# Kernel tuning notes

Measured on AMD Instinct MI355X. Metric: run time of the kernel, lower is better.

The kernel has to match this reference:

```python
import jax, jax.numpy as jnp
import numpy as np

B, S, D, H = 2, 2048, 1024, 16
HD = D // H          # 64
NREF = HD // 2       # 32 Householder reflections
BLOCK = 128          # flex_attention block granularity
ROPE_BASE = 10000.0


def setup_inputs() -> dict:
    key = jax.random.key(0)
    ks = jax.random.split(key, 12)
    x = jax.random.normal(ks[0], (B, S, D), jnp.float32)
    # block-causal block mask (flex_attention block_mask analogue)
    nb = S // BLOCK
    bm = jnp.tril(jnp.ones((nb, nb), bool))
    mask = jnp.repeat(jnp.repeat(bm, BLOCK, axis=0), BLOCK, axis=1)  # [S,S]
    s = lambda fan: fan ** -0.5
    vs = jax.random.normal(ks[1], (NREF, HD), jnp.float32) * 0.02
    w_qkv = jax.random.normal(ks[2], (D, 3 * D), jnp.float32) * s(D)
    w_out = jax.random.normal(ks[3], (D, D), jnp.float32) * s(D)
    w_gate = jax.random.normal(ks[4], (D, D), jnp.float32) * s(D)
    b_gate = jnp.zeros((D,), jnp.float32)
    w_mlp_gate = jax.random.normal(ks[5], (D, 8 * D), jnp.float32) * s(D)
    b_mlp_gate = jnp.zeros((8 * D,), jnp.float32)
    w_mlp_out = jax.random.normal(ks[6], (4 * D, D), jnp.float32) * s(4 * D)
    b_mlp_out = jnp.zeros((D,), jnp.float32)
    return dict(x=x, mask=mask, grid_size=S, vs=vs, w_qkv=w_qkv, w_out=w_out,
                w_gate=w_gate, b_gate=b_gate, w_mlp_gate=w_mlp_gate,
                b_mlp_gate=b_mlp_gate, w_mlp_out=w_mlp_out, b_mlp_out=b_mlp_out)


def rmsnorm(x):
    return x * jax.lax.rsqrt(jnp.mean(x * x, axis=-1, keepdims=True) + 1e-6)


def householder_matrix(vs):
    # Q = prod_i (I - 2 v_i v_i^T / |v_i|^2), applied sequentially as in torch loop
    def body(Q, v):
        vn = jnp.sum(v * v) + 1e-8
        return Q - (2.0 / vn) * jnp.outer(v, v @ Q), None
    Q0 = jnp.eye(HD, dtype=vs.dtype)
    Q, _ = jax.lax.scan(body, Q0, vs)
    return Q


def rope_tables(seq_len, dtype):
    inv_freq = 1.0 / (ROPE_BASE ** (jnp.arange(0, HD, 2, dtype=jnp.float32) / HD))
    ang = jnp.arange(seq_len, dtype=jnp.float32)[:, None] * inv_freq  # [S, HD/2]
    ang = jnp.concatenate([ang, ang], axis=-1)                        # [S, HD]
    return jnp.cos(ang).astype(dtype), jnp.sin(ang).astype(dtype)


def rotate_half(x):
    x1, x2 = jnp.split(x, 2, axis=-1)
    return jnp.concatenate([-x2, x1], axis=-1)


def reference(x, mask, grid_size, vs, w_qkv, w_out, w_gate, b_gate,
              w_mlp_gate, b_mlp_gate, w_mlp_out, b_mlp_out):
    del grid_size  # positions derived from sequence length
    resid = x
    h = rmsnorm(x)
    qkv = h @ w_qkv                                # [B,S,3D]
    q, k, v = jnp.split(qkv, 3, axis=-1)
    to_heads = lambda t: t.reshape(B, S, H, HD).transpose(0, 2, 1, 3)  # [B,H,S,hd]
    q, k, v = to_heads(q), to_heads(k), to_heads(v)

    # RnRoPE: inverse Householder rotation, rope, forward Householder rotation
    Q = householder_matrix(vs)                     # [hd,hd]
    q = q @ Q.T
    k = k @ Q.T
    cos, sin = rope_tables(S, x.dtype)             # [S,hd]
    cos = cos[None, None]; sin = sin[None, None]
    q = q * cos + rotate_half(q) * sin
    k = k * cos + rotate_half(k) * sin
    q = q @ Q
    k = k @ Q

    # block-sparse attention (mask realized as boolean [S,S])
    scores = jnp.einsum('bhqd,bhkd->bhqk', q, k) / jnp.sqrt(jnp.asarray(HD, x.dtype))
    scores = jnp.where(mask[None, None], scores, jnp.asarray(-1e30, x.dtype))
    attn = jnp.einsum('bhqk,bhkd->bhqd', jax.nn.softmax(scores, axis=-1), v)
    attn = attn.transpose(0, 2, 1, 3).reshape(B, S, D)
    attn = attn @ w_out

    gate = jax.nn.sigmoid(attn @ w_gate + b_gate)
    x = resid + attn * gate

    resid = x
    gv = rmsnorm(x) @ w_mlp_gate + b_mlp_gate      # [B,S,8D]
    g, val = jnp.split(gv, 2, axis=-1)
    x = resid + (val * jax.nn.gelu(g, approximate=False)) @ w_mlp_out + b_mlp_out
    return x
```

## Files before the change

### kernel.cpp

```cpp
#include <hip/hip_runtime.h>
#include <hip/hip_bf16.h>
#include <math.h>

#define BT 2
#define SEQ 2048
#define DIM 1024
#define NH 16
#define HD 64
#define NTOK (BT*SEQ)

typedef __attribute__((ext_vector_type(4))) float floatx4;
typedef __attribute__((ext_vector_type(8))) short shortx8;
typedef __attribute__((ext_vector_type(4))) short shortx4;

#define GLL16(gp, lp) __builtin_amdgcn_global_load_lds( \
    (const __attribute__((address_space(1))) unsigned int*)(const void*)(gp), \
    (__attribute__((address_space(3))) unsigned int*)(void*)(lp), 16, 0, 0)

__device__ __forceinline__ float bf2f(unsigned short u) {
    unsigned int x = ((unsigned int)u) << 16;
    return __builtin_bit_cast(float, x);
}
__device__ __forceinline__ unsigned short f2bf(float f) {
    unsigned int x = __builtin_bit_cast(unsigned int, f);
    unsigned int lsb = (x >> 16) & 1u;
    x += 0x7fffu + lsb;
    return (unsigned short)(x >> 16);
}
__device__ __forceinline__ float ldin_f(const void* p, size_t i, int isbf) {
    return isbf ? bf2f(((const unsigned short*)p)[i]) : ((const float*)p)[i];
}

__global__ void detect_kernel(const unsigned short* __restrict__ x, int* __restrict__ flag) {
    __shared__ int cnt;
    if (threadIdx.x == 0) cnt = 0;
    __syncthreads();
    unsigned short u = x[(size_t)threadIdx.x * 2];
    int e = (u >> 7) & 0xFF;
    if (e >= 100 && e <= 140) atomicAdd(&cnt, 1);
    __syncthreads();
    if (threadIdx.x == 0) *flag = (cnt >= 192) ? 1 : 0;
}

__global__ void transpose_any(const void* __restrict__ in,
                              unsigned short* __restrict__ out, int R, int C,
                              const int* __restrict__ flagp) {
    int isbf = *flagp;
    __shared__ unsigned short tile[32][33];
    int c0 = blockIdx.x * 32, r0 = blockIdx.y * 32;
    int tx = threadIdx.x, ty = threadIdx.y;
#pragma unroll
    for (int i = 0; i < 4; i++) {
        size_t idx = (size_t)(r0 + ty + i * 8) * C + c0 + tx;
        tile[ty + i * 8][tx] = isbf ? ((const unsigned short*)in)[idx]
                                    : f2bf(((const float*)in)[idx]);
    }
    __syncthreads();
#pragma unroll
    for (int i = 0; i < 4; i++)
        out[(size_t)(c0 + ty + i * 8) * R + r0 + tx] = tile[tx][ty + i * 8];
}

__global__ __launch_bounds__(64) void householder_kernel(const void* __restrict__ vs,
                                                         float* __restrict__ Qg,
                                                         const int* __restrict__ flagp) {
    int isbf = *flagp;
    __shared__ float vsh[64];
    int j = threadIdx.x;
    float Qc[64];
#pragma unroll
    for (int i = 0; i < 64; i++) Qc[i] = (i == j) ? 1.f : 0.f;
    for (int r = 0; r < 32; r++) {
        vsh[j] = ldin_f(vs, r * 64 + j, isbf);
        __syncthreads();
        float va[64];
#pragma unroll
        for (int i = 0; i < 64; i++) va[i] = vsh[i];
        float vn0 = 0.f, vn1 = 0.f, vn2 = 0.f, vn3 = 0.f;
        float t0 = 0.f, t1 = 0.f, t2 = 0.f, t3 = 0.f;
#pragma unroll
        for (int i = 0; i < 16; i++) {
            vn0 += va[4 * i + 0] * va[4 * i + 0];
            vn1 += va[4 * i + 1] * va[4 * i + 1];
            vn2 += va[4 * i + 2] * va[4 * i + 2];
            vn3 += va[4 * i + 3] * va[4 * i + 3];
            t0 += va[4 * i + 0] * Qc[4 * i + 0];
            t1 += va[4 * i + 1] * Qc[4 * i + 1];
            t2 += va[4 * i + 2] * Qc[4 * i + 2];
            t3 += va[4 * i + 3] * Qc[4 * i + 3];
        }
        float vn = (vn0 + vn1) + (vn2 + vn3) + 1e-8f;
        float t = (t0 + t1) + (t2 + t3);
        float c = (2.f / vn) * t;
#pragma unroll
        for (int i = 0; i < 64; i++) Qc[i] -= c * va[i];
        __syncthreads();
    }
#pragma unroll
    for (int i = 0; i < 64; i++) Qg[i * 64 + j] = Qc[i];
}

__global__ __launch_bounds__(256) void rotate_wqkv(unsigned short* __restrict__ wT,
                                                   const float* __restrict__ Qg) {
    __shared__ float Qs[64][64];
    __shared__ unsigned short tile[64][128];
    int bid = blockIdx.x;
    int row0 = (bid >> 3) * 64;
    int col0 = (bid & 7) * 128;
    int t = threadIdx.x;
#pragma unroll
    for (int i = 0; i < 16; i++) {
        int idx = i * 256 + t;
        Qs[idx >> 6][idx & 63] = Qg[idx];
    }
#pragma unroll
    for (int i = 0; i < 8; i++) {
        int e = i * 256 + t;
        int r = e >> 5, cg = (e & 31) * 4;
        *(shortx4*)&tile[r][cg] = *(const shortx4*)&wT[(size_t)(row0 + r) * 1024 + col0 + cg];
    }
    __syncthreads();
    int ib = t >> 5;
    int c = (t & 31) * 4;
    float acc[8][4];
#pragma unroll
    for (int rr = 0; rr < 8; rr++)
#pragma unroll
        for (int cx = 0; cx < 4; cx++) acc[rr][cx] = 0.f;
    for (int j = 0; j < 64; j++) {
        float t0 = bf2f(tile[j][c]);
        float t1 = bf2f(tile[j][c + 1]);
        float t2 = bf2f(tile[j][c + 2]);
        float t3 = bf2f(tile[j][c + 3]);
#pragma unroll
        for (int rr = 0; rr < 8; rr++) {
            float qv = Qs[rr * 8 + ib][j];
            acc[rr][0] += qv * t0;
            acc[rr][1] += qv * t1;
            acc[rr][2] += qv * t2;
            acc[rr][3] += qv * t3;
        }
    }
#pragma unroll
    for (int rr = 0; rr < 8; rr++) {
        int i = rr * 8 + ib;
        shortx4 o4;
#pragma unroll
        for (int cx = 0; cx < 4; cx++) o4[cx] = (short)f2bf(acc[rr][cx]);
        *(shortx4*)&wT[(size_t)(row0 + i) * 1024 + col0 + c] = o4;
    }
}

__global__ void rope_table(float* __restrict__ tab) {
    int idx = blockIdx.x * 256 + threadIdx.x;
    int s = idx >> 5, fi = idx & 31;
    float invf = __expf(-(float)fi * (9.210340371976184f / 32.f));
    float ang = (float)s * invf;
    tab[2 * idx]     = cosf(ang);
    tab[2 * idx + 1] = sinf(ang);
}

__global__ __launch_bounds__(256) void rmsnorm2(const void* __restrict__ x,
                                                unsigned short* __restrict__ h,
                                                const int* __restrict__ flagp) {
    int isbf = flagp ? *flagp : 1;
    __shared__ float red[256];
    int row = blockIdx.x, t = threadIdx.x;
    size_t base = (size_t)row * DIM;
    float v[4];
    float ss = 0.f;
#pragma unroll
    for (int i = 0; i < 4; i++) {
        v[i] = ldin_f(x, base + t + 256 * i, isbf);
        ss += v[i] * v[i];
    }
    red[t] = ss;
    __syncthreads();
    for (int s = 128; s > 0; s >>= 1) {
        if (t < s) red[t] += red[t + s];
        __syncthreads();
    }
    float rs = rsqrtf(red[0] * (1.f / 1024.f) + 1e-6f);
#pragma unroll
    for (int i = 0; i < 4; i++) h[base + t + 256 * i] = f2bf(v[i] * rs);
}

template<int BN>
__global__ __launch_bounds__(256) void gemm_bt(const unsigned short* __restrict__ A,
                                               const unsigned short* __restrict__ Bt,
                                               void* __restrict__ C,
                                               const void* __restrict__ bias,
                                               const unsigned short* __restrict__ resid,
                                               const int* __restrict__ flagp,
                                               int M, int N, int K, int c_f32) {
    constexpr int NJ = BN / 32;
    __shared__ __align__(16) unsigned short As[2][128][32];
    __shared__ __align__(16) unsigned short Bs[2][BN][32];
    int bisbf = (bias && flagp) ? *flagp : 1;
    int tile = (blockIdx.x & 7) * (gridDim.x >> 3) + (blockIdx.x >> 3);
    int nbn = N / BN;
    int m0 = (tile / nbn) * 128;
    int n0 = (tile % nbn) * BN;
    int t = threadIdx.x;
    int lane = t & 63;
    int w = t >> 6;
    int wr = (w >> 1) * 64;
    int wc = (w & 1) * (16 * NJ);
    int lr = lane & 15;
    int kg = lane >> 4;

    floatx4 acc[4][NJ];
#pragma unroll
    for (int i = 0; i < 4; i++)
#pragma unroll
        for (int j = 0; j < NJ; j++) acc[i][j] = (floatx4){0.f, 0.f, 0.f, 0.f};

    int srow = w * 16 + (lane >> 2);
    int skseg = (lane & 3) * 8;
    const unsigned short* aP = A + (size_t)(m0 + srow) * K + skseg;
    const unsigned short* bP = Bt + (size_t)(n0 + srow) * K + skseg;
    size_t r64 = (size_t)64 * K;

    GLL16(aP,       &As[0][w * 16][0]);
    GLL16(aP + r64, &As[0][64 + w * 16][0]);
    GLL16(bP,       &Bs[0][w * 16][0]);
    if constexpr (BN == 128) GLL16(bP + r64, &Bs[0][64 + w * 16][0]);
    __syncthreads();

    int cur = 0;
    for (int k0 = 0; k0 < K; k0 += 32) {
        if (k0 + 32 < K) {
            int nb = cur ^ 1;
            GLL16(aP + k0 + 32,       &As[nb][w * 16][0]);
            GLL16(aP + r64 + k0 + 32, &As[nb][64 + w * 16][0]);
            GLL16(bP + k0 + 32,       &Bs[nb][w * 16][0]);
            if constexpr (BN == 128) GLL16(bP + r64 + k0 + 32, &Bs[nb][64 + w * 16][0]);
        }
        shortx8 af[4], bfv[NJ];
#pragma unroll
        for (int i = 0; i < 4; i++) af[i] = *(const shortx8*)&As[cur][wr + i * 16 + lr][kg * 8];
#pragma unroll
        for (int j = 0; j < NJ; j++) bfv[j] = *(const shortx8*)&Bs[cur][wc + j * 16 + lr][kg * 8];
#pragma unroll
        for (int i = 0; i < 4; i++)
#pragma unroll
            for (int j = 0; j < NJ; j++)
                acc[i][j] = __builtin_amdgcn_mfma_f32_16x16x32_bf16(af[i], bfv[j], acc[i][j], 0, 0, 0);
        __syncthreads();
        cur ^= 1;
    }
#pragma unroll
    for (int i = 0; i < 4; i++) {
#pragma unroll
        for (int j = 0; j < NJ; j++) {
            int col = n0 + wc + j * 16 + lr;
            int rbase = m0 + wr + i * 16 + kg * 4;
            float bv = bias ? ldin_f(bias, col, bisbf) : 0.f;
#pragma unroll
            for (int r = 0; r < 4; r++) {
                float val = acc[i][j][r] + bv;
                size_t oidx = (size_t)(rbase + r) * N + col;
                if (resid) val += bf2f(resid[oidx]);
                if (c_f32) ((float*)C)[oidx] = val;
                else       ((unsigned short*)C)[oidx] = f2bf(val);
            }
        }
    }
}

__global__ __launch_bounds__(256) void gemm_glu(const unsigned short* __restrict__ A,
                                                const unsigned short* __restrict__ Bt,
                                                unsigned short* __restrict__ act,
                                                const void* __restrict__ bias,
                                                const int* __restrict__ flagp) {
    __shared__ __align__(16) unsigned short As[2][128][32];
    __shared__ __align__(16) unsigned short Bg[2][64][32];
    __shared__ __align__(16) unsigned short Bv[2][64][32];
    const int K = 1024;
    int isbf = *flagp;
    int tile = (blockIdx.x & 7) * (gridDim.x >> 3) + (blockIdx.x >> 3);
    int m0 = (tile & 31) * 128;
    int n0 = (tile >> 5) * 64;
    int t = threadIdx.x;
    int lane = t & 63;
    int w = t >> 6;
    int wr = (w >> 1) * 64;
    int wc = (w & 1) * 32;
    int lr = lane & 15;
    int kg = lane >> 4;

    floatx4 ag[4][2], av[4][2];
#pragma unroll
    for (int i = 0; i < 4; i++)
#pragma unroll
        for (int j = 0; j < 2; j++) {
            ag[i][j] = (floatx4){0.f, 0.f, 0.f, 0.f};
            av[i][j] = (floatx4){0.f, 0.f, 0.f, 0.f};
        }

    int srow = w * 16 + (lane >> 2);
    int skseg = (lane & 3) * 8;
    const unsigned short* aP  = A + (size_t)(m0 + srow) * K + skseg;
    const unsigned short* bgP = Bt + (size_t)(n0 + srow) * K + skseg;
    const unsigned short* bvP = Bt + (size_t)(4096 + n0 + srow) * K + skseg;
    size_t r64 = (size_t)64 * K;

    GLL16(aP,       &As[0][w * 16][0]);
    GLL16(aP + r64, &As[0][64 + w * 16][0]);
    GLL16(bgP,      &Bg[0][w * 16][0]);
    GLL16(bvP,      &Bv[0][w * 16][0]);
    __syncthreads();

    int cur = 0;
    for (int k0 = 0; k0 < K; k0 += 32) {
        if (k0 + 32 < K) {
            int nb = cur ^ 1;
            GLL16(aP + k0 + 32,       &As[nb][w * 16][0]);
            GLL16(aP + r64 + k0 + 32, &As[nb][64 + w * 16][0]);
            GLL16(bgP + k0 + 32,      &Bg[nb][w * 16][0]);
            GLL16(bvP + k0 + 32,      &Bv[nb][w * 16][0]);
        }
        shortx8 af[4], gf[2], vf[2];
#pragma unroll
        for (int i = 0; i < 4; i++) af[i] = *(const shortx8*)&As[cur][wr + i * 16 + lr][kg * 8];
#pragma unroll
        for (int j = 0; j < 2; j++) {
            gf[j] = *(const shortx8*)&Bg[cur][wc + j * 16 + lr][kg * 8];
            vf[j] = *(const shortx8*)&Bv[cur][wc + j * 16 + lr][kg * 8];
        }
#pragma unroll
        for (int i = 0; i < 4; i++)
#pragma unroll
            for (int j = 0; j < 2; j++) {
                ag[i][j] = __builtin_amdgcn_mfma_f32_16x16x32_bf16(af[i], gf[j], ag[i][j], 0, 0, 0);
                av[i][j] = __builtin_amdgcn_mfma_f32_16x16x32_bf16(af[i], vf[j], av[i][j], 0, 0, 0);
            }
        __syncthreads();
        cur ^= 1;
    }
#pragma unroll
    for (int i = 0; i < 4; i++) {
#pragma unroll
        for (int j = 0; j < 2; j++) {
            int col = n0 + wc + j * 16 + lr;
            int rbase = m0 + wr + i * 16 + kg * 4;
            float bgv = ldin_f(bias, col, isbf);
            float bvv = ldin_f(bias, 4096 + col, isbf);
#pragma unroll
            for (int r = 0; r < 4; r++) {
                float g = ag[i][j][r] + bgv;
                float v = av[i][j][r] + bvv;
                float ge = 0.5f * g * (1.f + erff(g * 0.70710678118f));
                act[(size_t)(rbase + r) * 4096 + col] = f2bf(v * ge);
            }
        }
    }
}

__global__ __launch_bounds__(256) void qk_rope3(const unsigned short* __restrict__ qkv,
                                                const float* __restrict__ tab,
                                                unsigned short* __restrict__ q_r,
                                                unsigned short* __restrict__ k_r) {
    int tid = blockIdx.x * 256 + threadIdx.x;
    int c = tid & 3;
    int h = (tid >> 2) & 15;
    int ts = tid >> 6;
    int s = ts & 2047, b = ts >> 11;
    int d0 = c * 8;
    const unsigned short* base = qkv + (size_t)ts * 3072 + h * 64;
    shortx8 qlo = *(const shortx8*)(base + d0);
    shortx8 qhi = *(const shortx8*)(base + d0 + 32);
    shortx8 klo = *(const shortx8*)(base + 1024 + d0);
    shortx8 khi = *(const shortx8*)(base + 1024 + d0 + 32);
    const float* tp = tab + (size_t)s * 64 + d0 * 2;
    shortx8 oql, oqh, okl, okh;
#pragma unroll
    for (int i = 0; i < 8; i++) {
        float cv = tp[2 * i], sv = tp[2 * i + 1];
        float ql = bf2f((unsigned short)qlo[i]), qh = bf2f((unsigned short)qhi[i]);
        float kl = bf2f((unsigned short)klo[i]), kh = bf2f((unsigned short)khi[i]);
        oql[i] = (short)f2bf(ql * cv - qh * sv);
        oqh[i] = (short)f2bf(qh * cv + ql * sv);
        okl[i] = (short)f2bf(kl * cv - kh * sv);
        okh[i] = (short)f2bf(kh * cv + kl * sv);
    }
    size_t o = ((size_t)(b * NH + h) * SEQ + s) * HD + d0;
    *(shortx8*)(q_r + o)      = oql;
    *(shortx8*)(q_r + o + 32) = oqh;
    *(shortx8*)(k_r + o)      = okl;
    *(shortx8*)(k_r + o + 32) = okh;
}

__global__ __launch_bounds__(512) void attn_mfma(const unsigned short* __restrict__ q_r,
                                                 const unsigned short* __restrict__ k_r,
                                                 const unsigned short* __restrict__ qkv,
                                                 unsigned short* __restrict__ attn) {
    __shared__ __align__(16) unsigned short Ks[64][72];
    __shared__ __align__(16) unsigned short Vt[64 * 72];
    __shared__ __align__(16) unsigned short Ps[8][16][72];
    int bid = blockIdx.x;
    int qblk = 15 - (bid & 15);
    int bh = bid >> 4;
    int b = bh >> 4, h = bh & 15;
    size_t bh_off = (size_t)bh * SEQ * HD;
    int tid = threadIdx.x;
    int wv = tid >> 6, lane = tid & 63;
    int l16 = lane & 15, quad = lane >> 4;
    int q0 = qblk * 128 + wv * 16;

    const unsigned short* qrow = q_r + bh_off + (size_t)(q0 + l16) * HD + quad * 8;
    shortx8 aq0 = *(const shortx8*)(qrow);
    shortx8 aq1 = *(const shortx8*)(qrow + 32);

    floatx4 o[4];
#pragma unroll
    for (int nt = 0; nt < 4; nt++) o[nt] = (floatx4){0.f, 0.f, 0.f, 0.f};
    float m_run = -1e30f, l_run = 0.f;

    int nk = (qblk + 1) * 128;
    int skey = tid >> 3;
    int sd0 = (tid & 7) * 8;
    const unsigned short* kbase = k_r + bh_off + (size_t)skey * HD + sd0;
    const unsigned short* vbase = qkv + ((size_t)(b * SEQ + skey)) * 3072 + 2048 + h * 64 + sd0;
    int vco = (((skey >> 3) ^ (tid & 7)) * 8) + (skey & 7);

    shortx8 kv = *(const shortx8*)kbase;
    shortx8 vvv = *(const shortx8*)vbase;

    for (int k0 = 0; k0 < nk; k0 += 64) {
        __syncthreads();
        *(shortx8*)&Ks[skey][sd0] = kv;
#pragma unroll
        for (int i = 0; i < 8; i++) Vt[(size_t)(sd0 + i) * 72 + vco] = (unsigned short)vvv[i];
        __syncthreads();
        if (k0 + 64 < nk) {
            kv  = *(const shortx8*)(kbase + (size_t)(k0 + 64) * HD);
            vvv = *(const shortx8*)(vbase + (size_t)(k0 + 64) * 3072);
        }

        floatx4 sc[4];
#pragma unroll
        for (int kt = 0; kt < 4; kt++) {
            shortx8 bk0 = *(const shortx8*)&Ks[kt * 16 + l16][quad * 8];
            shortx8 bk1 = *(const shortx8*)&Ks[kt * 16 + l16][32 + quad * 8];
            floatx4 z = (floatx4){0.f, 0.f, 0.f, 0.f};
            z = __builtin_amdgcn_mfma_f32_16x16x32_bf16(bk0, aq0, z, 0, 0, 0);
            z = __builtin_amdgcn_mfma_f32_16x16x32_bf16(bk1, aq1, z, 0, 0, 0);
            sc[kt] = z;
        }
        float sv[16], mx[16];
#pragma unroll
        for (int kt = 0; kt < 4; kt++)
#pragma unroll
            for (int r = 0; r < 4; r++) sv[kt * 4 + r] = sc[kt][r] * 0.125f;
#pragma unroll
        for (int i = 0; i < 16; i++) mx[i] = sv[i];
#pragma unroll
        for (int st = 8; st > 0; st >>= 1)
#pragma unroll
            for (int i = 0; i < 8; i++)
                if (i < st) mx[i] = fmaxf(mx[i], mx[i + st]);
        float mt = mx[0];
        mt = fmaxf(mt, __shfl_xor(mt, 16, 64));
        mt = fmaxf(mt, __shfl_xor(mt, 32, 64));
        float nm = fmaxf(m_run, mt);
        float al = __expf(m_run - nm);
        m_run = nm;
        float p[16];
#pragma unroll
        for (int i = 0; i < 16; i++) p[i] = __expf(sv[i] - nm);
        float sm[8];
#pragma unroll
        for (int i = 0; i < 8; i++) sm[i] = p[i] + p[i + 8];
        float ps = ((sm[0] + sm[1]) + (sm[2] + sm[3])) + ((sm[4] + sm[5]) + (sm[6] + sm[7]));
        ps += __shfl_xor(ps, 16, 64);
        ps += __shfl_xor(ps, 32, 64);
        l_run = l_run * al + ps;
#pragma unroll
        for (int kt = 0; kt < 4; kt++) {
            shortx4 pk;
#pragma unroll
            for (int r = 0; r < 4; r++) pk[r] = (short)f2bf(p[kt * 4 + r]);
            *(shortx4*)&Ps[wv][l16][kt * 16 + quad * 4] = pk;
        }
#pragma unroll
        for (int r = 0; r < 4; r++) {
            float alr = __shfl(al, quad * 4 + r, 64);
            o[0][r] *= alr; o[1][r] *= alr; o[2][r] *= alr; o[3][r] *= alr;
        }
#pragma unroll
        for (int h2 = 0; h2 < 2; h2++) {
            shortx8 ap = *(const shortx8*)&Ps[wv][l16][h2 * 32 + quad * 8];
#pragma unroll
            for (int nt = 0; nt < 4; nt++) {
                int dd = nt * 16 + l16;
                shortx8 bvv = *(const shortx8*)&Vt[(size_t)dd * 72 +
                                                   (((h2 * 4 + quad) ^ ((dd >> 3) & 7)) * 8)];
                o[nt] = __builtin_amdgcn_mfma_f32_16x16x32_bf16(ap, bvv, o[nt], 0, 0, 0);
            }
        }
    }
#pragma unroll
    for (int r = 0; r < 4; r++) {
        float lv = __shfl(l_run, quad * 4 + r, 64);
        float inv_l = 1.f / lv;
        int s = q0 + quad * 4 + r;
        unsigned short* op = attn + ((size_t)(b * SEQ + s)) * DIM + h * 64;
#pragma unroll
        for (int nt = 0; nt < 4; nt++) op[nt * 16 + l16] = f2bf(o[nt][r] * inv_l);
    }
}

__global__ void combine_gate(const void* __restrict__ x,
                             const unsigned short* __restrict__ ao,
                             const unsigned short* __restrict__ gl,
                             const void* __restrict__ bg,
                             unsigned short* __restrict__ x1,
                             const int* __restrict__ flagp) {
    int isbf = *flagp;
    size_t idx = (size_t)blockIdx.x * 256 + threadIdx.x;
    float a = bf2f(ao[idx]);
    float z = bf2f(gl[idx]) + ldin_f(bg, idx & 1023, isbf);
    float sg = 1.f / (1.f + __expf(-z));
    x1[idx] = f2bf(ldin_f(x, idx, isbf) + a * sg);
}

extern "C" void kernel_launch(void* const* d_in, const int* in_sizes, int n_in,
                              void* d_out, int out_size, void* d_ws, size_t ws_size,
                              hipStream_t stream) {
    const unsigned short* x        = (const unsigned short*)d_in[0];
    const void* vs       = d_in[3];
    const void* w_qkv    = d_in[4];
    const void* w_out    = d_in[5];
    const void* w_gate   = d_in[6];
    const void* b_gate   = d_in[7];
    const void* w_mlp_g  = d_in[8];
    const void* b_mlp_g  = d_in[9];
    const void* w_mlp_o  = d_in[10];
    const void* b_mlp_o  = d_in[11];
    float* out = (float*)d_out;
    char* ws = (char*)d_ws;

    if (n_in < 12) return;
    if (in_sizes[0] != 4194304 || in_sizes[3] != 2048 || in_sizes[4] != 3145728 ||
        in_sizes[8] != 8388608 || in_sizes[10] != 4194304 || in_sizes[7] != 1024) return;

    const size_t o_T   = 0;
    const size_t o_Qg  = 35651584;
    const size_t o_h   = 35684352;
    const size_t o_B   = 44072960;
    const size_t o_C   = 69238784;
    const size_t o_gv  = 94404608;
    const size_t total = 161513472;
    if (ws_size < total) return;

    unsigned short* wqkvT  = (unsigned short*)(ws + o_T);
    unsigned short* woutT  = (unsigned short*)(ws + o_T + 6291456);
    unsigned short* wgateT = (unsigned short*)(ws + o_T + 8388608);
    unsigned short* wmgT   = (unsigned short*)(ws + o_T + 10485760);
    unsigned short* wmoT   = (unsigned short*)(ws + o_T + 27262976);
    float*          Qg     = (float*)(ws + o_Qg);
    int*            flagp  = (int*)(ws + o_Qg + 16384);
    unsigned short* h      = (unsigned short*)(ws + o_h);
    unsigned short* qkv    = (unsigned short*)(ws + o_B);
    unsigned short* ao     = (unsigned short*)(ws + o_B + 8388608);
    unsigned short* gl     = (unsigned short*)(ws + o_B + 16777216);
    unsigned short* q_rb   = (unsigned short*)(ws + o_C);
    unsigned short* k_rb   = (unsigned short*)(ws + o_C + 8388608);
    unsigned short* attnb  = (unsigned short*)(ws + o_C + 16777216);
    unsigned short* x1     = (unsigned short*)(ws + o_C);
    unsigned short* act    = (unsigned short*)(ws + o_C + 8388608);
    float*          rtab   = (float*)(ws + o_gv);

    detect_kernel<<<1, 256, 0, stream>>>(x, flagp);
    householder_kernel<<<1, 64, 0, stream>>>(vs, Qg, flagp);
    rope_table<<<256, 256, 0, stream>>>(rtab);

    dim3 tb(32, 8);
    transpose_any<<<dim3(3072 / 32, 1024 / 32), tb, 0, stream>>>(w_qkv,   wqkvT, 1024, 3072, flagp);
    transpose_any<<<dim3(1024 / 32, 1024 / 32), tb, 0, stream>>>(w_out,   woutT, 1024, 1024, flagp);
    transpose_any<<<dim3(1024 / 32, 1024 / 32), tb, 0, stream>>>(w_gate,  wgateT, 1024, 1024, flagp);
    transpose_any<<<dim3(8192 / 32, 1024 / 32), tb, 0, stream>>>(w_mlp_g, wmgT, 1024, 8192, flagp);
    transpose_any<<<dim3(1024 / 32, 4096 / 32), tb, 0, stream>>>(w_mlp_o, wmoT, 4096, 1024, flagp);
    rotate_wqkv<<<256, 256, 0, stream>>>(wqkvT, Qg);

    rmsnorm2<<<NTOK, 256, 0, stream>>>(x, h, flagp);
    gemm_bt<128><<<32 * 24, 256, 0, stream>>>(h, wqkvT, qkv, nullptr, nullptr, flagp, NTOK, 3072, 1024, 0);
    qk_rope3<<<1024, 256, 0, stream>>>(qkv, rtab, q_rb, k_rb);
    attn_mfma<<<BT * NH * (SEQ / 128), 512, 0, stream>>>(q_rb, k_rb, qkv, attnb);
    gemm_bt<64><<<32 * 16, 256, 0, stream>>>(attnb, woutT, ao, nullptr, nullptr, flagp, NTOK, 1024, 1024, 0);
    gemm_bt<64><<<32 * 16, 256, 0, stream>>>(ao, wgateT, gl, nullptr, nullptr, flagp, NTOK, 1024, 1024, 0);
    combine_gate<<<NTOK * DIM / 256, 256, 0, stream>>>(x, ao, gl, b_gate, x1, flagp);
    rmsnorm2<<<NTOK, 256, 0, stream>>>(x1, h, nullptr);
    gemm_glu<<<32 * 64, 256, 0, stream>>>(h, wmgT, act, b_mlp_g, flagp);
    gemm_bt<64><<<32 * 16, 256, 0, stream>>>(act, wmoT, (void*)out, b_mlp_o, x1, flagp, NTOK, 1024, 4096, 1);
}
```

Baseline: 576.8 us.

## Deepen GEMM prefetch with explicit vmcnt waits and fuse gate epilogue

Replaces the GEMM and GLU main loops' double-buffer-plus-__syncthreads scheme with a two-stage-ahead prefetch. Each async global-to-LDS load is issued right after the compute barrier, and partial vmcnt waits plus raw s_barrier calls keep one stage of loads in flight while computing. The sigmoid-gate combine kernel is folded into the gate GEMM epilogue, so the intermediate gate-logit buffer and one elementwise launch go away. The hand-written waitcnt and barrier sequence raises the risk of races if the counts do not match the loads in flight.

```diff
diff --git a/kernel.cpp b/kernel.cpp
--- a/kernel.cpp
+++ b/kernel.cpp
@@ -16,6 +16,17 @@
 #define GLL16(gp, lp) __builtin_amdgcn_global_load_lds( \
     (const __attribute__((address_space(1))) unsigned int*)(const void*)(gp), \
     (__attribute__((address_space(3))) unsigned int*)(void*)(lp), 16, 0, 0)
+
+template<int N> __device__ __forceinline__ void waitvm() {
+    if constexpr (N == 0) asm volatile("s_waitcnt vmcnt(0)" ::: "memory");
+    else if constexpr (N == 3) asm volatile("s_waitcnt vmcnt(3)" ::: "memory");
+    else if constexpr (N == 4) asm volatile("s_waitcnt vmcnt(4)" ::: "memory");
+}
+__device__ __forceinline__ void barrier_raw() {
+    asm volatile("" ::: "memory");
+    __builtin_amdgcn_s_barrier();
+    asm volatile("" ::: "memory");
+}
 
 __device__ __forceinline__ float bf2f(unsigned short u) {
     unsigned int x = ((unsigned int)u) << 16;
@@ -185,18 +196,20 @@
     for (int i = 0; i < 4; i++) h[base + t + 256 * i] = f2bf(v[i] * rs);
 }
 
-template<int BN>
+template<int BN, int MODE>
 __global__ __launch_bounds__(256) void gemm_bt(const unsigned short* __restrict__ A,
                                                const unsigned short* __restrict__ Bt,
                                                void* __restrict__ C,
                                                const void* __restrict__ bias,
                                                const unsigned short* __restrict__ resid,
+                                               const void* __restrict__ xin,
                                                const int* __restrict__ flagp,
-                                               int M, int N, int K, int c_f32) {
+                                               int M, int N, int K) {
     constexpr int NJ = BN / 32;
+    constexpr int NLD = (BN == 128) ? 4 : 3;
     __shared__ __align__(16) unsigned short As[2][128][32];
     __shared__ __align__(16) unsigned short Bs[2][BN][32];
-    int bisbf = (bias && flagp) ? *flagp : 1;
+    int isbf = flagp ? *flagp : 1;
     int tile = (blockIdx.x & 7) * (gridDim.x >> 3) + (blockIdx.x >> 3);
     int nbn = N / BN;
     int m0 = (tile / nbn) * 128;
@@ -221,21 +234,22 @@
     const unsigned short* bP = Bt + (size_t)(n0 + srow) * K + skseg;
     size_t r64 = (size_t)64 * K;
 
-    GLL16(aP,       &As[0][w * 16][0]);
-    GLL16(aP + r64, &As[0][64 + w * 16][0]);
-    GLL16(bP,       &Bs[0][w * 16][0]);
-    if constexpr (BN == 128) GLL16(bP + r64, &Bs[0][64 + w * 16][0]);
-    __syncthreads();
+    auto STAGE = [&](int s, int b) {
+        int off = s * 32;
+        GLL16(aP + off,       &As[b][w * 16][0]);
+        GLL16(aP + r64 + off, &As[b][64 + w * 16][0]);
+        GLL16(bP + off,       &Bs[b][w * 16][0]);
+        if constexpr (BN == 128) GLL16(bP + r64 + off, &Bs[b][64 + w * 16][0]);
+    };
+
+    int NS = K / 32;
+    STAGE(0, 0);
+    STAGE(1, 1);
+    waitvm<NLD>();
+    barrier_raw();
 
     int cur = 0;
-    for (int k0 = 0; k0 < K; k0 += 32) {
-        if (k0 + 32 < K) {
-            int nb = cur ^ 1;
-            GLL16(aP + k0 + 32,       &As[nb][w * 16][0]);
-            GLL16(aP + r64 + k0 + 32, &As[nb][64 + w * 16][0]);
-            GLL16(bP + k0 + 32,       &Bs[nb][w * 16][0]);
-            if constexpr (BN == 128) GLL16(bP + r64 + k0 + 32, &Bs[nb][64 + w * 16][0]);
-        }
+    for (int s = 0; s < NS; ++s) {
         shortx8 af[4], bfv[NJ];
 #pragma unroll
         for (int i = 0; i < 4; i++) af[i] = *(const shortx8*)&As[cur][wr + i * 16 + lr][kg * 8];
@@ -246,7 +260,15 @@
 #pragma unroll
             for (int j = 0; j < NJ; j++)
                 acc[i][j] = __builtin_amdgcn_mfma_f32_16x16x32_bf16(af[i], bfv[j], acc[i][j], 0, 0, 0);
-        __syncthreads();
+        barrier_raw();
+        if (s + 2 < NS) {
+            STAGE(s + 2, cur);
+            waitvm<NLD>();
+            barrier_raw();
+        } else if (s + 1 < NS) {
+            waitvm<0>();
+            barrier_raw();
+        }
         cur ^= 1;
     }
 #pragma unroll
@@ -255,14 +277,20 @@
         for (int j = 0; j < NJ; j++) {
             int col = n0 + wc + j * 16 + lr;
             int rbase = m0 + wr + i * 16 + kg * 4;
-            float bv = bias ? ldin_f(bias, col, bisbf) : 0.f;
+            float bv = bias ? ldin_f(bias, col, isbf) : 0.f;
 #pragma unroll
             for (int r = 0; r < 4; r++) {
                 float val = acc[i][j][r] + bv;
                 size_t oidx = (size_t)(rbase + r) * N + col;
-                if (resid) val += bf2f(resid[oidx]);
-                if (c_f32) ((float*)C)[oidx] = val;
-                else       ((unsigned short*)C)[oidx] = f2bf(val);
+                if constexpr (MODE == 0) {
+                    ((unsigned short*)C)[oidx] = f2bf(val);
+                } else if constexpr (MODE == 1) {
+                    ((float*)C)[oidx] = val + bf2f(resid[oidx]);
+                } else {
+                    float a = bf2f(resid[oidx]);
+                    float sg = 1.f / (1.f + __expf(-val));
+                    ((unsigned short*)C)[oidx] = f2bf(ldin_f(xin, oidx, isbf) + a * sg);
+                }
             }
         }
     }
@@ -305,21 +333,22 @@
     const unsigned short* bvP = Bt + (size_t)(4096 + n0 + srow) * K + skseg;
     size_t r64 = (size_t)64 * K;
 
-    GLL16(aP,       &As[0][w * 16][0]);
-    GLL16(aP + r64, &As[0][64 + w * 16][0]);
-    GLL16(bgP,      &Bg[0][w * 16][0]);
-    GLL16(bvP,      &Bv[0][w * 16][0]);
-    __syncthreads();
+    auto STAGE = [&](int s, int b) {
+        int off = s * 32;
+        GLL16(aP + off,       &As[b][w * 16][0]);
+        GLL16(aP + r64 + off, &As[b][64 + w * 16][0]);
+        GLL16(bgP + off,      &Bg[b][w * 16][0]);
+        GLL16(bvP + off,      &Bv[b][w * 16][0]);
+    };
+
+    const int NS = K / 32;
+    STAGE(0, 0);
+    STAGE(1, 1);
+    waitvm<4>();
+    barrier_raw();
 
     int cur = 0;
-    for (int k0 = 0; k0 < K; k0 += 32) {
-        if (k0 + 32 < K) {
-            int nb = cur ^ 1;
-            GLL16(aP + k0 + 32,       &As[nb][w * 16][0]);
-            GLL16(aP + r64 + k0 + 32, &As[nb][64 + w * 16][0]);
-            GLL16(bgP + k0 + 32,      &Bg[nb][w * 16][0]);
-            GLL16(bvP + k0 + 32,      &Bv[nb][w * 16][0]);
-        }
+    for (int s = 0; s < NS; ++s) {
         shortx8 af[4], gf[2], vf[2];
 #pragma unroll
         for (int i = 0; i < 4; i++) af[i] = *(const shortx8*)&As[cur][wr + i * 16 + lr][kg * 8];
@@ -335,7 +364,15 @@
                 ag[i][j] = __builtin_amdgcn_mfma_f32_16x16x32_bf16(af[i], gf[j], ag[i][j], 0, 0, 0);
                 av[i][j] = __builtin_amdgcn_mfma_f32_16x16x32_bf16(af[i], vf[j], av[i][j], 0, 0, 0);
             }
-        __syncthreads();
+        barrier_raw();
+        if (s + 2 < NS) {
+            STAGE(s + 2, cur);
+            waitvm<4>();
+            barrier_raw();
+        } else if (s + 1 < NS) {
+            waitvm<0>();
+            barrier_raw();
+        }
         cur ^= 1;
     }
 #pragma unroll
@@ -511,20 +548,6 @@
     }
 }
 
-__global__ void combine_gate(const void* __restrict__ x,
-                             const unsigned short* __restrict__ ao,
-                             const unsigned short* __restrict__ gl,
-                             const void* __restrict__ bg,
-                             unsigned short* __restrict__ x1,
-                             const int* __restrict__ flagp) {
-    int isbf = *flagp;
-    size_t idx = (size_t)blockIdx.x * 256 + threadIdx.x;
-    float a = bf2f(ao[idx]);
-    float z = bf2f(gl[idx]) + ldin_f(bg, idx & 1023, isbf);
-    float sg = 1.f / (1.f + __expf(-z));
-    x1[idx] = f2bf(ldin_f(x, idx, isbf) + a * sg);
-}
-
 extern "C" void kernel_launch(void* const* d_in, const int* in_sizes, int n_in,
                               void* d_out, int out_size, void* d_ws, size_t ws_size,
                               hipStream_t stream) {
@@ -564,7 +587,6 @@
     unsigned short* h      = (unsigned short*)(ws + o_h);
     unsigned short* qkv    = (unsigned short*)(ws + o_B);
     unsigned short* ao     = (unsigned short*)(ws + o_B + 8388608);
-    unsigned short* gl     = (unsigned short*)(ws + o_B + 16777216);
     unsigned short* q_rb   = (unsigned short*)(ws + o_C);
     unsigned short* k_rb   = (unsigned short*)(ws + o_C + 8388608);
     unsigned short* attnb  = (unsigned short*)(ws + o_C + 16777216);
@@ -585,13 +607,12 @@
     rotate_wqkv<<<256, 256, 0, stream>>>(wqkvT, Qg);
 
     rmsnorm2<<<NTOK, 256, 0, stream>>>(x, h, flagp);
-    gemm_bt<128><<<32 * 24, 256, 0, stream>>>(h, wqkvT, qkv, nullptr, nullptr, flagp, NTOK, 3072, 1024, 0);
+    gemm_bt<128, 0><<<32 * 24, 256, 0, stream>>>(h, wqkvT, qkv, nullptr, nullptr, nullptr, flagp, NTOK, 3072, 1024);
     qk_rope3<<<1024, 256, 0, stream>>>(qkv, rtab, q_rb, k_rb);
     attn_mfma<<<BT * NH * (SEQ / 128), 512, 0, stream>>>(q_rb, k_rb, qkv, attnb);
-    gemm_bt<64><<<32 * 16, 256, 0, stream>>>(attnb, woutT, ao, nullptr, nullptr, flagp, NTOK, 1024, 1024, 0);
-    gemm_bt<64><<<32 * 16, 256, 0, stream>>>(ao, wgateT, gl, nullptr, nullptr, flagp, NTOK, 1024, 1024, 0);
-    combine_gate<<<NTOK * DIM / 256, 256, 0, stream>>>(x, ao, gl, b_gate, x1, flagp);
+    gemm_bt<64, 0><<<32 * 16, 256, 0, stream>>>(attnb, woutT, ao, nullptr, nullptr, nullptr, flagp, NTOK, 1024, 1024);
+    gemm_bt<64, 2><<<32 * 16, 256, 0, stream>>>(ao, wgateT, x1, b_gate, ao, x, flagp, NTOK, 1024, 1024);
     rmsnorm2<<<NTOK, 256, 0, stream>>>(x1, h, nullptr);
     gemm_glu<<<32 * 64, 256, 0, stream>>>(h, wmgT, act, b_mlp_g, flagp);
-    gemm_bt<64><<<32 * 16, 256, 0, stream>>>(act, wmoT, (void*)out, b_mlp_o, x1, flagp, NTOK, 1024, 4096, 1);
-}
+    gemm_bt<64, 1><<<32 * 16, 256, 0, stream>>>(act, wmoT, (void*)out, b_mlp_o, x1, nullptr, flagp, NTOK, 1024, 4096);
+}
```

After: 565.1 us. 2.0% less time.
